# Optimization experiments

Hardware: AMD Instinct MI355X
Metric: run time of the kernel (lower is better)

## Reference

```python
import jax, jax.numpy as jnp
import numpy as np

NUM_HEADS = 8
BLOCK_SIZE = 32   # tokens per block
WINDOW = 64       # window radius in blocks -> attends to blocks [i-64, i+64]


def setup_inputs() -> dict:
    key = jax.random.key(0)
    ks = jax.random.split(key, 5)
    B, N, C = 8, 8192, 512
    s = 0.02
    return {
        "x": jax.random.normal(ks[0], (B, N, C), dtype=jnp.float32),
        # torch Linear(dim, 3*dim): y = x @ W.T + b; we store W already transposed [in, out]
        "W_qkv": jax.random.normal(ks[1], (C, 3 * C), dtype=jnp.float32) * s,
        "b_qkv": jax.random.normal(ks[2], (3 * C,), dtype=jnp.float32) * s,
        "W_proj": jax.random.normal(ks[3], (C, C), dtype=jnp.float32) * s,
        "b_proj": jax.random.normal(ks[4], (C,), dtype=jnp.float32) * s,
    }


def reference(x, W_qkv, b_qkv, W_proj, b_proj):
    B, N, C = x.shape
    h = NUM_HEADS
    dh = C // h
    scale = jnp.asarray(dh, x.dtype) ** -0.5

    # qkv projection, then the module's head-interleaved split:
    # rearrange 'b n (h d) -> b h n d' with d = 3C/h, chunk(3) on last dim,
    # rearrange back 'b h n d -> b n (h d)'. Equivalent to:
    qkv = (x @ W_qkv + b_qkv).reshape(B, N, h, 3 * dh)
    q = qkv[..., :dh].reshape(B, N, C)
    k = qkv[..., dh:2 * dh].reshape(B, N, C)
    v = qkv[..., 2 * dh:].reshape(B, N, C)

    # dynamic blocking (N chosen divisible by BLOCK_SIZE -> no padding)
    nb = N // BLOCK_SIZE
    qb = q.reshape(B, nb, BLOCK_SIZE, C)
    kb = k.reshape(B, nb, BLOCK_SIZE, C)
    vb = v.reshape(B, nb, BLOCK_SIZE, C)

    # per-offset block attention: query block i, position s attends to
    # position s of every block j in [i-WINDOW, i+WINDOW]
    attn = jnp.einsum('bisc,bjsc->bisj', qb, kb) * scale  # [B, nb, s, nb]
    i_idx = jnp.arange(nb)[:, None]
    j_idx = jnp.arange(nb)[None, :]
    band = (j_idx >= i_idx - WINDOW) & (j_idx <= i_idx + WINDOW)  # [nb, nb]
    neg = jnp.finfo(attn.dtype).min
    attn = jnp.where(band[None, :, None, :], attn, neg)
    attn = jax.nn.softmax(attn, axis=-1)
    out = jnp.einsum('bisj,bjsc->bisc', attn, vb)  # [B, nb, s, C]
    out = out.reshape(B, N, C)

    # 'b n (h d) -> b n h d -> b n (h d)' is the identity
    return out @ W_proj + b_proj
```

## Files before the change

kernel.cpp:

```cpp
#include <hip/hip_runtime.h>
#include <hip/hip_bf16.h>
#include <stdint.h>

#define B_   8
#define N_   8192
#define C_   512
#define NB   256
#define WIN  64

typedef __attribute__((ext_vector_type(8))) short short8;
typedef __attribute__((ext_vector_type(4))) float f32x4;
typedef __hip_bfloat16 bf16;

__device__ __forceinline__ void gload_lds16(const void* g, void* l) {
  __builtin_amdgcn_global_load_lds((const __attribute__((address_space(1))) void*)g,
                                   (__attribute__((address_space(3))) void*)l, 16, 0, 0);
}

__device__ __forceinline__ f32x4 mfma16(short8 a, short8 b, f32x4 c) {
  return __builtin_amdgcn_mfma_f32_16x16x32_bf16(a, b, c, 0, 0, 0);
}


__global__ __launch_bounds__(256) void k_conv_x(const float4* __restrict__ x,
                                                ushort4* __restrict__ xb) {
  size_t idx = (size_t)blockIdx.x * 256 + threadIdx.x;
  float4 v = x[idx];
  union { ushort4 u; bf16 b[4]; } o;
  o.b[0] = __float2bfloat16(v.x); o.b[1] = __float2bfloat16(v.y);
  o.b[2] = __float2bfloat16(v.z); o.b[3] = __float2bfloat16(v.w);
  xb[idx] = o.u;
}

__global__ __launch_bounds__(256) void k_conv_w(const float* __restrict__ W,
                                                const float* __restrict__ bsrc,
                                                bf16* __restrict__ Wt,
                                                float* __restrict__ bperm,
                                                int ldw, int qkv) {
  __shared__ float tile[32][65];
  const int cc = blockIdx.x, k0 = blockIdx.y * 32;
  const int src0 = cc * 64;
  const int o0 = qkv ? ((cc % 3) * 512 + (cc / 3) * 64) : src0;
  const int tid = threadIdx.x;
#pragma unroll
  for (int q = 0; q < 8; ++q) {
    int li = q * 256 + tid;
    int r = li >> 6, c = li & 63;
    tile[r][c] = W[(size_t)(k0 + r) * ldw + src0 + c];
  }
  __syncthreads();
#pragma unroll
  for (int q = 0; q < 8; ++q) {
    int li = q * 256 + tid;
    int c2 = li >> 5, kk = li & 31;
    Wt[(size_t)(o0 + c2) * 512 + k0 + kk] = __float2bfloat16(tile[kk][c2]);
  }
  if (qkv && blockIdx.y == 0 && tid < 64) bperm[o0 + tid] = bsrc[src0 + tid];
}

#define WAITV(N) asm volatile("s_waitcnt vmcnt(" #N ")" ::: "memory")

template <int EPI>
__global__ __launch_bounds__(512, 2) void k_gemm(const bf16* __restrict__ A,
                                                 const bf16* __restrict__ Bt,
                                                 const float* __restrict__ bias,
                                                 bf16* __restrict__ qb,
                                                 bf16* __restrict__ kb,
                                                 bf16* __restrict__ vb,
                                                 float* __restrict__ outf,
                                                 int NT) {
  extern __shared__ char gsm[];
  const int tid = threadIdx.x;
  const int lane = tid & 63, wid = tid >> 6;
  const int wr = wid >> 2, wcn = wid & 3;
  const int l15 = lane & 15, l4 = lane >> 4;
  const int sx = l15 & 7;

  const int nwg = gridDim.x;
  const int cpx = nwg >> 3;
  const int swz = (blockIdx.x & 7) * cpx + (blockIdx.x >> 3);
  const int mt = swz / NT, nt = swz % NT;
  const size_t m0 = (size_t)mt * 256;
  const int n0 = nt * 256;

  f32x4 acc[8][4];
#pragma unroll
  for (int fi = 0; fi < 8; ++fi)
#pragma unroll
    for (int fj = 0; fj < 4; ++fj) acc[fi][fj] = (f32x4){0.f, 0.f, 0.f, 0.f};

#define STAGE_A(E, H, K0)                                                      \
  { _Pragma("unroll") for (int q = 0; q < 2; ++q) {                            \
      int li = q * 512 + tid;                                                  \
      int r = li >> 3, g = (li & 7) ^ (r & 7);                                 \
      gload_lds16(A + (m0 + (H) * 128 + r) * 512 + (K0) + g * 8,               \
                  gsm + (E) * 65536 + (H) * 16384 + li * 16);                  \
    } }
#define STAGE_B(E, H, K0)                                                      \
  { _Pragma("unroll") for (int q = 0; q < 2; ++q) {                            \
      int li = q * 512 + tid;                                                  \
      int r = li >> 3, g = (li & 7) ^ (r & 7);                                 \
      gload_lds16(Bt + (size_t)(n0 + (H) * 128 + r) * 512 + (K0) + g * 8,      \
                  gsm + (E) * 65536 + 32768 + (H) * 16384 + li * 16);          \
    } }

#define PHASE(FIH, FJH, LOADA, STAGE_STMT, WAIT_STMT)                          \
  {                                                                            \
    const char* Ab = gsm + d * 65536 + (FIH) * 16384;                          \
    const char* Bb = gsm + d * 65536 + 32768 + (FJH) * 16384;                  \
    if (LOADA) {                                                               \
      _Pragma("unroll") for (int f = 0; f < 4; ++f) {                          \
        int rA = f * 32 + wr * 16 + l15;                                       \
        af[f][0] = *(const short8*)(Ab + rA * 128 + ((l4 ^ sx) << 4));         \
        af[f][1] = *(const short8*)(Ab + rA * 128 + (((4 + l4) ^ sx) << 4));   \
      }                                                                        \
    }                                                                          \
    _Pragma("unroll") for (int f = 0; f < 2; ++f) {                            \
      int rB = f * 64 + wcn * 16 + l15;                                        \
      bfr[f][0] = *(const short8*)(Bb + rB * 128 + ((l4 ^ sx) << 4));          \
      bfr[f][1] = *(const short8*)(Bb + rB * 128 + (((4 + l4) ^ sx) << 4));    \
    }                                                                          \
    STAGE_STMT;                                                                \
    __builtin_amdgcn_sched_barrier(0);                                         \
    __builtin_amdgcn_s_barrier();                                              \
    __builtin_amdgcn_sched_barrier(0);                                         \
    __builtin_amdgcn_s_setprio(1);                                             \
    _Pragma("unroll") for (int f = 0; f < 4; ++f)                              \
      _Pragma("unroll") for (int g = 0; g < 2; ++g) {                          \
        acc[(FIH) * 4 + f][(FJH) * 2 + g] =                                    \
            mfma16(af[f][0], bfr[g][0], acc[(FIH) * 4 + f][(FJH) * 2 + g]);    \
        acc[(FIH) * 4 + f][(FJH) * 2 + g] =                                    \
            mfma16(af[f][1], bfr[g][1], acc[(FIH) * 4 + f][(FJH) * 2 + g]);    \
      }                                                                        \
    __builtin_amdgcn_s_setprio(0);                                             \
    __builtin_amdgcn_sched_barrier(0);                                         \
    WAIT_STMT;                                                                 \
    __builtin_amdgcn_s_barrier();                                              \
  }

  STAGE_A(0, 0, 0); STAGE_B(0, 0, 0); STAGE_B(0, 1, 0); STAGE_A(0, 1, 0);
  WAITV(4);
  __builtin_amdgcn_s_barrier();

  short8 af[4][2], bfr[2][2];
  for (int t = 0; t < 8; ++t) {
    const int d = t & 1, e = d ^ 1;
    const int kn = (t + 1) * 64;
    PHASE(0, 0, 1,
          { if (t < 7) STAGE_A(e, 0, kn); },
          { if (t < 7) { WAITV(4); } else { WAITV(2); } });
    PHASE(0, 1, 0,
          { if (t < 7) STAGE_B(e, 0, kn); },
          { if (t < 7) { WAITV(4); } else { WAITV(0); } });
    PHASE(1, 0, 1,
          { if (t < 7) STAGE_B(e, 1, kn); },
          { });
    PHASE(1, 1, 0,
          { if (t < 7) STAGE_A(e, 1, kn); },
          { if (t < 7) { WAITV(4); } });
  }
#undef PHASE
#undef STAGE_A
#undef STAGE_B

  if (EPI == 0) {
#pragma unroll
    for (int fi = 0; fi < 8; ++fi)
#pragma unroll
      for (int fj = 0; fj < 4; ++fj) {
        int o = n0 + fj * 64 + wcn * 16 + l15;
        float bia = bias[o];
        int part = o >> 9;
        int c = o & 511;
        bf16* dst = part == 0 ? qb : (part == 1 ? kb : vb);
#pragma unroll
        for (int r = 0; r < 4; ++r) {
          size_t m = m0 + fi * 32 + wr * 16 + l4 * 4 + r;
          int bidx = (int)(m >> 13);
          int n = (int)(m & 8191);
          int blk = n >> 5, s = n & 31;
          size_t di = (((size_t)(bidx * 32 + s) * 256 + blk) << 9) | c;
          dst[di] = __float2bfloat16(acc[fi][fj][r] + bia);
        }
      }
  } else {
#pragma unroll
    for (int fi = 0; fi < 8; ++fi)
#pragma unroll
      for (int fj = 0; fj < 4; ++fj) {
        int o = n0 + fj * 64 + wcn * 16 + l15;
        float bia = bias[o];
#pragma unroll
        for (int r = 0; r < 4; ++r) {
          size_t m = m0 + fi * 32 + wr * 16 + l4 * 4 + r;
          outf[m * 512 + o] = acc[fi][fj][r] + bia;
        }
      }
  }
}

__global__ __launch_bounds__(256) void k_transpose_v(const bf16* __restrict__ v,
                                                     bf16* __restrict__ vT) {
  __shared__ bf16 t[32][36];
  int bs = blockIdx.x, j0 = blockIdx.y * 32, c0 = blockIdx.z * 32;
  const bf16* src = v + (size_t)bs * NB * C_;
  bf16* dst = vT + (size_t)bs * C_ * NB;
  int r = threadIdx.x >> 3, c4 = (threadIdx.x & 7) * 4;
  *(ushort4*)&t[r][c4] = *(const ushort4*)(src + (size_t)(j0 + r) * C_ + c0 + c4);
  __syncthreads();
  union { ushort4 u; bf16 b[4]; } o;
  o.b[0] = t[c4 + 0][r]; o.b[1] = t[c4 + 1][r];
  o.b[2] = t[c4 + 2][r]; o.b[3] = t[c4 + 3][r];
  *(ushort4*)(dst + (size_t)(c0 + r) * NB + j0 + c4) = o.u;
}

#define KB_OFF   0
#define VB_OFF   65536
#define SS_OFF   98304
#define PS_OFF   102528
#define MR_OFF   105088
#define LR_OFF   105216
#define AL_OFF   105344
#define ATTN_LDS 105472

__global__ __launch_bounds__(512) void k_attn(const bf16* __restrict__ qg,
                                              const bf16* __restrict__ kg,
                                              const bf16* __restrict__ vTg,
                                              bf16* __restrict__ outb) {
  extern __shared__ char smc[];
  float* Ssf  = (float*)(smc + SS_OFF);
  bf16*  Psb  = (bf16*)(smc + PS_OFF);
  float* mrow = (float*)(smc + MR_OFF);
  float* lrow = (float*)(smc + LR_OFF);
  float* alph = (float*)(smc + AL_OFF);

  const int tid = threadIdx.x, lane = tid & 63, wid = tid >> 6;
  const int l15 = lane & 15, l4 = lane >> 4;
  const int gt = (blockIdx.x & 7) * 256 + (blockIdx.x >> 3);
  const int bs = gt >> 3;
  const int b = bs >> 5, s = bs & 31;
  const int i0 = (gt & 7) * 32;
  const int jlo = max(0, i0 - WIN);
  const int jhi = min(NB - 1, i0 + 31 + WIN);
  const int nch = (jhi - jlo + 1) >> 5;
  const bf16* Qb = qg + (size_t)bs * NB * C_;
  const bf16* Kb = kg + (size_t)bs * NB * C_;
  const bf16* Vb = vTg + (size_t)bs * C_ * NB;

  const int qhq = wid & 1, jhq = (wid >> 1) & 1;
  const int qh_pv = wid >> 2, cq = wid & 3;

  f32x4 O[8];
#pragma unroll
  for (int f = 0; f < 8; ++f) O[f] = (f32x4){0.f, 0.f, 0.f, 0.f};

  if (tid < 32) { mrow[tid] = -1e30f; lrow[tid] = 0.f; }

#pragma unroll
  for (int q = 0; q < 4; ++q) {
    int li = q * 512 + tid;
    int row = li >> 6, g = (li & 63) ^ (row & 15);
    gload_lds16(Kb + (size_t)(jlo + row) * C_ + g * 8, smc + KB_OFF + li * 16);
  }
  short8 qreg[16];
  if (wid < 4) {
    const bf16* qp = Qb + (size_t)(i0 + qhq * 16 + l15) * C_ + l4 * 8;
#pragma unroll
    for (int cc = 0; cc < 16; ++cc)
      qreg[cc] = *(const short8*)(qp + cc * 32);
  }

  for (int t = 0; t < nch; ++t) {
    const int j0 = jlo + t * 32;
    asm volatile("s_waitcnt lgkmcnt(0)" ::: "memory");
    __builtin_amdgcn_s_barrier();
    __builtin_amdgcn_sched_barrier(0);

#pragma unroll
    for (int q = 0; q < 4; ++q) {
      int li = q * 512 + tid;
      int c = li >> 2, g = (li & 3) ^ (c & 3);
      gload_lds16(Vb + (size_t)c * NB + j0 + g * 8, smc + VB_OFF + li * 16);
    }
    if (t + 1 < nch) {
      int jn = j0 + 32;
      char* kdst = smc + KB_OFF + ((t + 1) & 1) * 32768;
#pragma unroll
      for (int q = 0; q < 4; ++q) {
        int li = q * 512 + tid;
        int row = li >> 6, g = (li & 63) ^ (row & 15);
        gload_lds16(Kb + (size_t)(jn + row) * C_ + g * 8, kdst + li * 16);
      }
      asm volatile("s_waitcnt vmcnt(8)" ::: "memory");
    } else {
      asm volatile("s_waitcnt vmcnt(4)" ::: "memory");
    }
    __builtin_amdgcn_s_barrier();
    __builtin_amdgcn_sched_barrier(0);

    if (wid < 4) {
      const int brow = jhq * 16 + l15;
      const char* Kbase = smc + KB_OFF + (t & 1) * 32768 + brow * 1024;
      f32x4 a0 = (f32x4){0.f, 0.f, 0.f, 0.f}, a1 = a0;
      __builtin_amdgcn_s_setprio(1);
#pragma unroll
      for (int cc = 0; cc < 16; ++cc) {
        int sb = (cc * 4 + l4) ^ (brow & 15);
        short8 bv = *(const short8*)(Kbase + sb * 16);
        if (cc & 1) a1 = mfma16(qreg[cc], bv, a1);
        else        a0 = mfma16(qreg[cc], bv, a0);
      }
      __builtin_amdgcn_s_setprio(0);
      f32x4 su = a0 + a1;
      int jg = j0 + jhq * 16 + l15;
#pragma unroll
      for (int r = 0; r < 4; ++r) {
        int i_in = qhq * 16 + l4 * 4 + r;
        int i_abs = i0 + i_in;
        bool valid = (jg >= i_abs - WIN) && (jg <= i_abs + WIN);
        Ssf[i_in * 33 + jhq * 16 + l15] = valid ? su[r] * 0.125f : -1e30f;
      }
    }
    asm volatile("s_waitcnt lgkmcnt(0)" ::: "memory");
    __builtin_amdgcn_s_barrier();
    __builtin_amdgcn_sched_barrier(0);

    {
      int row = tid >> 4, u = tid & 15;
      float s0 = Ssf[row * 33 + u], s1 = Ssf[row * 33 + u + 16];
      float mc = fmaxf(s0, s1);
      mc = fmaxf(mc, __shfl_xor(mc, 1));
      mc = fmaxf(mc, __shfl_xor(mc, 2));
      mc = fmaxf(mc, __shfl_xor(mc, 4));
      mc = fmaxf(mc, __shfl_xor(mc, 8));
      float mo = mrow[row];
      float mn = fmaxf(mo, mc);
      float a = __expf(mo - mn);
      float p0 = __expf(s0 - mn), p1 = __expf(s1 - mn);
      float ps = p0 + p1;
      ps += __shfl_xor(ps, 1);
      ps += __shfl_xor(ps, 2);
      ps += __shfl_xor(ps, 4);
      ps += __shfl_xor(ps, 8);
      if (u == 0) {
        lrow[row] = lrow[row] * a + ps;
        mrow[row] = mn;
        alph[row] = a;
      }
      Psb[row * 40 + u] = __float2bfloat16(p0);
      Psb[row * 40 + u + 16] = __float2bfloat16(p1);
    }
    if (t + 1 < nch)
      asm volatile("s_waitcnt vmcnt(4) lgkmcnt(0)" ::: "memory");
    else
      asm volatile("s_waitcnt vmcnt(0) lgkmcnt(0)" ::: "memory");
    __builtin_amdgcn_s_barrier();
    __builtin_amdgcn_sched_barrier(0);

    {
      float ar[4];
#pragma unroll
      for (int r = 0; r < 4; ++r) ar[r] = alph[qh_pv * 16 + l4 * 4 + r];
      short8 pa = *(const short8*)(smc + PS_OFF + (qh_pv * 16 + l15) * 80 + l4 * 16);
      __builtin_amdgcn_s_setprio(1);
#pragma unroll
      for (int f = 0; f < 8; ++f) {
        int c = cq * 128 + f * 16 + l15;
        short8 vv = *(const short8*)(smc + VB_OFF + c * 64 + ((l4 ^ (c & 3)) << 4));
#pragma unroll
        for (int r = 0; r < 4; ++r) O[f][r] *= ar[r];
        O[f] = mfma16(pa, vv, O[f]);
      }
      __builtin_amdgcn_s_setprio(0);
    }
    __builtin_amdgcn_sched_barrier(0);
  }

  asm volatile("s_waitcnt lgkmcnt(0)" ::: "memory");
  __builtin_amdgcn_s_barrier();
  {
    float lr[4];
#pragma unroll
    for (int r = 0; r < 4; ++r) lr[r] = 1.f / lrow[qh_pv * 16 + l4 * 4 + r];
#pragma unroll
    for (int f = 0; f < 8; ++f) {
      int c = cq * 128 + f * 16 + l15;
#pragma unroll
      for (int r = 0; r < 4; ++r) {
        int il = qh_pv * 16 + l4 * 4 + r;
        int n = (i0 + il) * 32 + s;
        outb[((size_t)b * N_ + n) * C_ + c] = __float2bfloat16(O[f][r] * lr[r]);
      }
    }
  }
}

extern "C" void kernel_launch(void* const* d_in, const int* in_sizes, int n_in,
                              void* d_out, int out_size, void* d_ws, size_t ws_size,
                              hipStream_t stream) {
  const float* x = (const float*)d_in[0];
  const float* Wqkv = (const float*)d_in[1];
  const float* bqkv = (const float*)d_in[2];
  const float* Wproj = (const float*)d_in[3];
  const float* bproj = (const float*)d_in[4];

  char* ws = (char*)d_ws;
  const size_t SLOT = 67108864ull;
  bf16* slotA = (bf16*)ws;
  bf16* slotB = (bf16*)(ws + SLOT);
  bf16* Wqkv_t = (bf16*)(ws + 2 * SLOT);
  bf16* Wproj_t = (bf16*)(ws + 2 * SLOT + 1572864);
  float* bias_perm = (float*)(ws + 2 * SLOT + 1572864 + 524288);
  bf16* qbuf = (bf16*)d_out;
  bf16* kbuf = qbuf + 33554432ull;

  static int attr_done = 0;
  if (!attr_done) {
    hipFuncSetAttribute((const void*)k_gemm<0>,
                        hipFuncAttributeMaxDynamicSharedMemorySize, 131072);
    hipFuncSetAttribute((const void*)k_gemm<1>,
                        hipFuncAttributeMaxDynamicSharedMemorySize, 131072);
    hipFuncSetAttribute((const void*)k_attn,
                        hipFuncAttributeMaxDynamicSharedMemorySize, ATTN_LDS);
    attr_done = 1;
  }

  k_conv_x<<<32768, 256, 0, stream>>>((const float4*)x, (ushort4*)slotA);
  k_conv_w<<<dim3(24, 16), 256, 0, stream>>>(Wqkv, bqkv, Wqkv_t, bias_perm, 1536, 1);
  k_conv_w<<<dim3(8, 16), 256, 0, stream>>>(Wproj, nullptr, Wproj_t, nullptr, 512, 0);

  k_gemm<0><<<1536, 512, 131072, stream>>>(slotA, Wqkv_t, bias_perm,
                                           qbuf, kbuf, slotB, nullptr, 6);
  k_transpose_v<<<dim3(256, 8, 16), 256, 0, stream>>>(slotB, slotA);
  k_attn<<<2048, 512, ATTN_LDS, stream>>>(qbuf, kbuf, slotA, slotB);
  k_gemm<1><<<512, 512, 131072, stream>>>(slotB, Wproj_t, bproj,
                                          nullptr, nullptr, nullptr, (float*)d_out, 2);
}
```

Measured before the change: 334.6 us.

## Make GEMM kernels persistent, prefetching the next tile during the current tile

Both GEMM launches now use 256 workgroups, each looping over several consecutive 256x256 output tiles. The first K-slice of the next tile is staged into LDS during the last K step of the current tile, so load latency at tile boundaries overlaps with compute. Tile order changes from the swizzled mapping to M-fastest within a workgroup's contiguous range, which alters L2 reuse of the B operand. The epilogue now runs inside the loop while the prefetch is in flight.

```diff
diff --git a/kernel.cpp b/kernel.cpp
--- a/kernel.cpp
+++ b/kernel.cpp
@@ -68,7 +68,7 @@
                                                  bf16* __restrict__ kb,
                                                  bf16* __restrict__ vb,
                                                  float* __restrict__ outf,
-                                                 int NT) {
+                                                 int NTL) {
   extern __shared__ char gsm[];
   const int tid = threadIdx.x;
   const int lane = tid & 63, wid = tid >> 6;
@@ -76,31 +76,20 @@
   const int l15 = lane & 15, l4 = lane >> 4;
   const int sx = l15 & 7;
 
-  const int nwg = gridDim.x;
-  const int cpx = nwg >> 3;
-  const int swz = (blockIdx.x & 7) * cpx + (blockIdx.x >> 3);
-  const int mt = swz / NT, nt = swz % NT;
-  const size_t m0 = (size_t)mt * 256;
-  const int n0 = nt * 256;
-
-  f32x4 acc[8][4];
-#pragma unroll
-  for (int fi = 0; fi < 8; ++fi)
-#pragma unroll
-    for (int fj = 0; fj < 4; ++fj) acc[fi][fj] = (f32x4){0.f, 0.f, 0.f, 0.f};
-
-#define STAGE_A(E, H, K0)                                                      \
+  const int T0 = blockIdx.x * NTL;
+
+#define STAGE_A(E, H, K0, M0)                                                  \
   { _Pragma("unroll") for (int q = 0; q < 2; ++q) {                            \
       int li = q * 512 + tid;                                                  \
       int r = li >> 3, g = (li & 7) ^ (r & 7);                                 \
-      gload_lds16(A + (m0 + (H) * 128 + r) * 512 + (K0) + g * 8,               \
+      gload_lds16(A + ((M0) + (H) * 128 + r) * 512 + (K0) + g * 8,             \
                   gsm + (E) * 65536 + (H) * 16384 + li * 16);                  \
     } }
-#define STAGE_B(E, H, K0)                                                      \
+#define STAGE_B(E, H, K0, N0)                                                  \
   { _Pragma("unroll") for (int q = 0; q < 2; ++q) {                            \
       int li = q * 512 + tid;                                                  \
       int r = li >> 3, g = (li & 7) ^ (r & 7);                                 \
-      gload_lds16(Bt + (size_t)(n0 + (H) * 128 + r) * 512 + (K0) + g * 8,      \
+      gload_lds16(Bt + (size_t)((N0) + (H) * 128 + r) * 512 + (K0) + g * 8,    \
                   gsm + (E) * 65536 + 32768 + (H) * 16384 + li * 16);          \
     } }
 
@@ -138,65 +127,88 @@
     __builtin_amdgcn_s_barrier();                                              \
   }
 
-  STAGE_A(0, 0, 0); STAGE_B(0, 0, 0); STAGE_B(0, 1, 0); STAGE_A(0, 1, 0);
+  {
+    const size_t m0p = (size_t)(T0 & 255) * 256;
+    const int n0p = (T0 >> 8) * 256;
+    STAGE_A(0, 0, 0, m0p); STAGE_B(0, 0, 0, n0p);
+    STAGE_B(0, 1, 0, n0p); STAGE_A(0, 1, 0, m0p);
+  }
   WAITV(4);
   __builtin_amdgcn_s_barrier();
 
+  f32x4 acc[8][4];
   short8 af[4][2], bfr[2][2];
-  for (int t = 0; t < 8; ++t) {
-    const int d = t & 1, e = d ^ 1;
-    const int kn = (t + 1) * 64;
-    PHASE(0, 0, 1,
-          { if (t < 7) STAGE_A(e, 0, kn); },
-          { if (t < 7) { WAITV(4); } else { WAITV(2); } });
-    PHASE(0, 1, 0,
-          { if (t < 7) STAGE_B(e, 0, kn); },
-          { if (t < 7) { WAITV(4); } else { WAITV(0); } });
-    PHASE(1, 0, 1,
-          { if (t < 7) STAGE_B(e, 1, kn); },
-          { });
-    PHASE(1, 1, 0,
-          { if (t < 7) STAGE_A(e, 1, kn); },
-          { if (t < 7) { WAITV(4); } });
+
+  for (int i = 0; i < NTL; ++i) {
+    const int T = T0 + i;
+    const size_t m0 = (size_t)(T & 255) * 256;
+    const int n0 = (T >> 8) * 256;
+    const size_t m0n = (size_t)((T + 1) & 255) * 256;
+    const int n0n = ((T + 1) >> 8) * 256;
+
+#pragma unroll
+    for (int fi = 0; fi < 8; ++fi)
+#pragma unroll
+      for (int fj = 0; fj < 4; ++fj) acc[fi][fj] = (f32x4){0.f, 0.f, 0.f, 0.f};
+
+    for (int t = 0; t < 8; ++t) {
+      const int d = t & 1, e = d ^ 1;
+      const bool more = (t < 7) || (i + 1 < NTL);
+      const int kn = (t < 7) ? (t + 1) * 64 : 0;
+      const size_t ma = (t < 7) ? m0 : m0n;
+      const int nb = (t < 7) ? n0 : n0n;
+      PHASE(0, 0, 1,
+            { if (more) STAGE_A(e, 0, kn, ma); },
+            { if (more) { WAITV(4); } else { WAITV(2); } });
+      PHASE(0, 1, 0,
+            { if (more) STAGE_B(e, 0, kn, nb); },
+            { if (more) { WAITV(4); } else { WAITV(0); } });
+      PHASE(1, 0, 1,
+            { if (more) STAGE_B(e, 1, kn, nb); },
+            { });
+      PHASE(1, 1, 0,
+            { if (more) STAGE_A(e, 1, kn, ma); },
+            { if (more) { WAITV(4); } });
+    }
+
+    if (EPI == 0) {
+#pragma unroll
+      for (int fi = 0; fi < 8; ++fi)
+#pragma unroll
+        for (int fj = 0; fj < 4; ++fj) {
+          int o = n0 + fj * 64 + wcn * 16 + l15;
+          float bia = bias[o];
+          int part = o >> 9;
+          int c = o & 511;
+          bf16* dst = part == 0 ? qb : (part == 1 ? kb : vb);
+#pragma unroll
+          for (int r = 0; r < 4; ++r) {
+            size_t m = m0 + fi * 32 + wr * 16 + l4 * 4 + r;
+            int bidx = (int)(m >> 13);
+            int n = (int)(m & 8191);
+            int blk = n >> 5, s = n & 31;
+            size_t di = (((size_t)(bidx * 32 + s) * 256 + blk) << 9) | c;
+            dst[di] = __float2bfloat16(acc[fi][fj][r] + bia);
+          }
+        }
+    } else {
+#pragma unroll
+      for (int fi = 0; fi < 8; ++fi)
+#pragma unroll
+        for (int fj = 0; fj < 4; ++fj) {
+          int o = n0 + fj * 64 + wcn * 16 + l15;
+          float bia = bias[o];
+#pragma unroll
+          for (int r = 0; r < 4; ++r) {
+            size_t m = m0 + fi * 32 + wr * 16 + l4 * 4 + r;
+            outf[m * 512 + o] = acc[fi][fj][r] + bia;
+          }
+        }
+    }
   }
 #undef PHASE
 #undef STAGE_A
 #undef STAGE_B
-
-  if (EPI == 0) {
-#pragma unroll
-    for (int fi = 0; fi < 8; ++fi)
-#pragma unroll
-      for (int fj = 0; fj < 4; ++fj) {
-        int o = n0 + fj * 64 + wcn * 16 + l15;
-        float bia = bias[o];
-        int part = o >> 9;
-        int c = o & 511;
-        bf16* dst = part == 0 ? qb : (part == 1 ? kb : vb);
-#pragma unroll
-        for (int r = 0; r < 4; ++r) {
-          size_t m = m0 + fi * 32 + wr * 16 + l4 * 4 + r;
-          int bidx = (int)(m >> 13);
-          int n = (int)(m & 8191);
-          int blk = n >> 5, s = n & 31;
-          size_t di = (((size_t)(bidx * 32 + s) * 256 + blk) << 9) | c;
-          dst[di] = __float2bfloat16(acc[fi][fj][r] + bia);
-        }
-      }
-  } else {
-#pragma unroll
-    for (int fi = 0; fi < 8; ++fi)
-#pragma unroll
-      for (int fj = 0; fj < 4; ++fj) {
-        int o = n0 + fj * 64 + wcn * 16 + l15;
-        float bia = bias[o];
-#pragma unroll
-        for (int r = 0; r < 4; ++r) {
-          size_t m = m0 + fi * 32 + wr * 16 + l4 * 4 + r;
-          outf[m * 512 + o] = acc[fi][fj][r] + bia;
-        }
-      }
-  }
 }
 
 __global__ __launch_bounds__(256) void k_transpose_v(const bf16* __restrict__ v,
@@ -429,10 +441,10 @@
   k_conv_w<<<dim3(24, 16), 256, 0, stream>>>(Wqkv, bqkv, Wqkv_t, bias_perm, 1536, 1);
   k_conv_w<<<dim3(8, 16), 256, 0, stream>>>(Wproj, nullptr, Wproj_t, nullptr, 512, 0);
 
-  k_gemm<0><<<1536, 512, 131072, stream>>>(slotA, Wqkv_t, bias_perm,
-                                           qbuf, kbuf, slotB, nullptr, 6);
+  k_gemm<0><<<256, 512, 131072, stream>>>(slotA, Wqkv_t, bias_perm,
+                                          qbuf, kbuf, slotB, nullptr, 6);
   k_transpose_v<<<dim3(256, 8, 16), 256, 0, stream>>>(slotB, slotA);
   k_attn<<<2048, 512, ATTN_LDS, stream>>>(qbuf, kbuf, slotA, slotB);
-  k_gemm<1><<<512, 512, 131072, stream>>>(slotB, Wproj_t, bproj,
+  k_gemm<1><<<256, 512, 131072, stream>>>(slotB, Wproj_t, bproj,
                                           nullptr, nullptr, nullptr, (float*)d_out, 2);
 }
```

Measured after the change: 339.1 us. No clear change (+1.3%).

## Split QK^T over all eight waves and drop K double-buffering for two blocks per CU

Applied to the files above, without the earlier changes.

The QK^T stage now runs on all eight waves instead of four. Each wave pair splits the 512-wide reduction in half and combines its partial sums through a new LDS reduction buffer and an extra barrier. K double-buffering is removed, so K and V are both loaded at the start of each chunk with a full vmcnt(0) wait. These changes shrink LDS from about 105KB to 77KB and halve the Q register footprint, which together with launch_bounds(512,2) aims for two workgroups per CU. In exchange, prefetch overlap is lost and there is an extra synchronization per chunk.

```diff
diff --git a/kernel.cpp b/kernel.cpp
--- a/kernel.cpp
+++ b/kernel.cpp
@@ -215,21 +215,23 @@
 }
 
 #define KB_OFF   0
-#define VB_OFF   65536
-#define SS_OFF   98304
-#define PS_OFF   102528
-#define MR_OFF   105088
-#define LR_OFF   105216
-#define AL_OFF   105344
-#define ATTN_LDS 105472
-
-__global__ __launch_bounds__(512) void k_attn(const bf16* __restrict__ qg,
-                                              const bf16* __restrict__ kg,
-                                              const bf16* __restrict__ vTg,
-                                              bf16* __restrict__ outb) {
+#define VB_OFF   32768
+#define SS_OFF   65536
+#define PS_OFF   69760
+#define SR_OFF   72320
+#define MR_OFF   76416
+#define LR_OFF   76544
+#define AL_OFF   76672
+#define ATTN_LDS 76800
+
+__global__ __launch_bounds__(512, 2) void k_attn(const bf16* __restrict__ qg,
+                                                 const bf16* __restrict__ kg,
+                                                 const bf16* __restrict__ vTg,
+                                                 bf16* __restrict__ outb) {
   extern __shared__ char smc[];
   float* Ssf  = (float*)(smc + SS_OFF);
   bf16*  Psb  = (bf16*)(smc + PS_OFF);
+  float* Sred = (float*)(smc + SR_OFF);
   float* mrow = (float*)(smc + MR_OFF);
   float* lrow = (float*)(smc + LR_OFF);
   float* alph = (float*)(smc + AL_OFF);
@@ -247,7 +249,7 @@
   const bf16* Kb = kg + (size_t)bs * NB * C_;
   const bf16* Vb = vTg + (size_t)bs * C_ * NB;
 
-  const int qhq = wid & 1, jhq = (wid >> 1) & 1;
+  const int qhq = (wid >> 2) & 1, jhq = (wid >> 1) & 1, ksq = wid & 1;
   const int qh_pv = wid >> 2, cq = wid & 3;
 
   f32x4 O[8];
@@ -256,17 +258,11 @@
 
   if (tid < 32) { mrow[tid] = -1e30f; lrow[tid] = 0.f; }
 
-#pragma unroll
-  for (int q = 0; q < 4; ++q) {
-    int li = q * 512 + tid;
-    int row = li >> 6, g = (li & 63) ^ (row & 15);
-    gload_lds16(Kb + (size_t)(jlo + row) * C_ + g * 8, smc + KB_OFF + li * 16);
-  }
-  short8 qreg[16];
-  if (wid < 4) {
-    const bf16* qp = Qb + (size_t)(i0 + qhq * 16 + l15) * C_ + l4 * 8;
-#pragma unroll
-    for (int cc = 0; cc < 16; ++cc)
+  short8 qreg[8];
+  {
+    const bf16* qp = Qb + (size_t)(i0 + qhq * 16 + l15) * C_ + ksq * 256 + l4 * 8;
+#pragma unroll
+    for (int cc = 0; cc < 8; ++cc)
       qreg[cc] = *(const short8*)(qp + cc * 32);
   }
 
@@ -279,51 +275,54 @@
 #pragma unroll
     for (int q = 0; q < 4; ++q) {
       int li = q * 512 + tid;
+      int row = li >> 6, g = (li & 63) ^ (row & 15);
+      gload_lds16(Kb + (size_t)(j0 + row) * C_ + g * 8, smc + KB_OFF + li * 16);
+    }
+#pragma unroll
+    for (int q = 0; q < 4; ++q) {
+      int li = q * 512 + tid;
       int c = li >> 2, g = (li & 3) ^ (c & 3);
       gload_lds16(Vb + (size_t)c * NB + j0 + g * 8, smc + VB_OFF + li * 16);
     }
-    if (t + 1 < nch) {
-      int jn = j0 + 32;
-      char* kdst = smc + KB_OFF + ((t + 1) & 1) * 32768;
-#pragma unroll
-      for (int q = 0; q < 4; ++q) {
-        int li = q * 512 + tid;
-        int row = li >> 6, g = (li & 63) ^ (row & 15);
-        gload_lds16(Kb + (size_t)(jn + row) * C_ + g * 8, kdst + li * 16);
-      }
-      asm volatile("s_waitcnt vmcnt(8)" ::: "memory");
-    } else {
-      asm volatile("s_waitcnt vmcnt(4)" ::: "memory");
-    }
+    asm volatile("s_waitcnt vmcnt(0)" ::: "memory");
     __builtin_amdgcn_s_barrier();
     __builtin_amdgcn_sched_barrier(0);
 
-    if (wid < 4) {
+    {
       const int brow = jhq * 16 + l15;
-      const char* Kbase = smc + KB_OFF + (t & 1) * 32768 + brow * 1024;
+      const char* Kbase = smc + KB_OFF + brow * 1024;
       f32x4 a0 = (f32x4){0.f, 0.f, 0.f, 0.f}, a1 = a0;
       __builtin_amdgcn_s_setprio(1);
 #pragma unroll
-      for (int cc = 0; cc < 16; ++cc) {
-        int sb = (cc * 4 + l4) ^ (brow & 15);
+      for (int cc = 0; cc < 8; ++cc) {
+        int sb = (ksq * 32 + cc * 4 + l4) ^ (brow & 15);
         short8 bv = *(const short8*)(Kbase + sb * 16);
         if (cc & 1) a1 = mfma16(qreg[cc], bv, a1);
         else        a0 = mfma16(qreg[cc], bv, a0);
       }
       __builtin_amdgcn_s_setprio(0);
-      f32x4 su = a0 + a1;
-      int jg = j0 + jhq * 16 + l15;
-#pragma unroll
-      for (int r = 0; r < 4; ++r) {
-        int i_in = qhq * 16 + l4 * 4 + r;
-        int i_abs = i0 + i_in;
-        bool valid = (jg >= i_abs - WIN) && (jg <= i_abs + WIN);
-        Ssf[i_in * 33 + jhq * 16 + l15] = valid ? su[r] * 0.125f : -1e30f;
-      }
-    }
-    asm volatile("s_waitcnt lgkmcnt(0)" ::: "memory");
-    __builtin_amdgcn_s_barrier();
-    __builtin_amdgcn_sched_barrier(0);
+      f32x4 acc = a0 + a1;
+      if (ksq) {
+        *(f32x4*)&Sred[(wid >> 1) * 256 + lane * 4] = acc;
+      }
+      asm volatile("s_waitcnt lgkmcnt(0)" ::: "memory");
+      __builtin_amdgcn_s_barrier();
+      __builtin_amdgcn_sched_barrier(0);
+      if (!ksq) {
+        f32x4 su = acc + *(f32x4*)&Sred[(wid >> 1) * 256 + lane * 4];
+        int jg = j0 + jhq * 16 + l15;
+#pragma unroll
+        for (int r = 0; r < 4; ++r) {
+          int i_in = qhq * 16 + l4 * 4 + r;
+          int i_abs = i0 + i_in;
+          bool valid = (jg >= i_abs - WIN) && (jg <= i_abs + WIN);
+          Ssf[i_in * 33 + jhq * 16 + l15] = valid ? su[r] * 0.125f : -1e30f;
+        }
+      }
+      asm volatile("s_waitcnt lgkmcnt(0)" ::: "memory");
+      __builtin_amdgcn_s_barrier();
+      __builtin_amdgcn_sched_barrier(0);
+    }
 
     {
       int row = tid >> 4, u = tid & 15;
@@ -350,10 +349,7 @@
       Psb[row * 40 + u] = __float2bfloat16(p0);
       Psb[row * 40 + u + 16] = __float2bfloat16(p1);
     }
-    if (t + 1 < nch)
-      asm volatile("s_waitcnt vmcnt(4) lgkmcnt(0)" ::: "memory");
-    else
-      asm volatile("s_waitcnt vmcnt(0) lgkmcnt(0)" ::: "memory");
+    asm volatile("s_waitcnt lgkmcnt(0)" ::: "memory");
     __builtin_amdgcn_s_barrier();
     __builtin_amdgcn_sched_barrier(0);
 
```

Result: no change. 340.1 us (+1.7%).
